# Optimization experiments

Measured on AMD Instinct MI355X. Metric: run time of the kernel, lower is better.

Reference implementation:

```python
import jax, jax.numpy as jnp
import numpy as np

IN_FEATURES = 4096
OUT_FEATURES = 11008
GROUPSIZE = 128


def setup_inputs() -> dict:
    key = jax.random.key(0)
    k_x, k_w, k_s, k_z = jax.random.split(key, 4)
    x = jax.random.normal(k_x, (4, 2048, IN_FEATURES), dtype=jnp.float32)
    # each int32 word packs 8 int4 nibbles along the in_features axis
    packed_weight = jax.random.randint(
        k_w, (IN_FEATURES // 8, OUT_FEATURES), 0, 2147483647, dtype=jnp.int32
    )
    n_groups = IN_FEATURES // GROUPSIZE
    scales = jax.random.uniform(k_s, (OUT_FEATURES, n_groups), dtype=jnp.float32)
    zeros = jax.random.uniform(k_z, (OUT_FEATURES, n_groups), dtype=jnp.float32)
    return {
        "x": x,
        "packed_weight": packed_weight,
        "scales": scales,
        "zeros": zeros,
        "groupsize": GROUPSIZE,
    }


def reference(x, packed_weight, scales, zeros, groupsize):
    # Unpack int4 nibbles: element i of in_features lives in packed_weight[i//8],
    # nibble (i % 8) (little-endian nibble order).
    in_features = packed_weight.shape[0] * 8
    shifts = (jnp.arange(8, dtype=jnp.int32) * 4)  # [8]
    q = (packed_weight[:, None, :] >> shifts[None, :, None]) & 0xF  # [in//8, 8, out]
    q = q.reshape(in_features, -1).astype(jnp.float32)  # [in, out]
    # Per-group dequant: w = (q - zero) * scale, groups along in_features.
    s = jnp.repeat(scales.T, groupsize, axis=0)  # [in, out]
    z = jnp.repeat(zeros.T, groupsize, axis=0)   # [in, out]
    w = (q - z) * s
    return jnp.einsum("bsi,io->bso", x, w)
```

## Files before the change

kernel.cpp:

```cpp
#include <hip/hip_runtime.h>


#define M_DIM 8192
#define K_DIM 4096
#define N_DIM 11008
#define BM 256
#define BN 256
#define BK 64
#define NKT (K_DIM / BK)

typedef unsigned short u16;
typedef __bf16 bf16x8 __attribute__((ext_vector_type(8)));
typedef float floatx4 __attribute__((ext_vector_type(4)));
typedef u16 u16x8 __attribute__((ext_vector_type(8)));
typedef u16 u16x4 __attribute__((ext_vector_type(4)));

typedef __attribute__((address_space(1))) const void* gcvp;
typedef __attribute__((address_space(3))) void* svp;

static __device__ __forceinline__ u16 f2b(float f) {
  union { float f; unsigned u; } v;
  v.f = f;
  unsigned r = v.u + 0x7FFFu + ((v.u >> 16) & 1u);
  return (u16)(r >> 16);
}

__global__ __launch_bounds__(256) void cvt_x_kernel(const float* __restrict__ x,
                                                    u16* __restrict__ xb) {
  int i = blockIdx.x * 256 + threadIdx.x;
  const int n4 = (M_DIM * K_DIM) / 4;
  const int stride = 2048 * 256;
  for (; i < n4; i += stride) {
    const float4 v = reinterpret_cast<const float4*>(x)[i];
    u16x4 r;
    r[0] = f2b(v.x); r[1] = f2b(v.y); r[2] = f2b(v.z); r[3] = f2b(v.w);
    reinterpret_cast<u16x4*>(xb)[i] = r;
  }
}

__global__ __launch_bounds__(256) void dequant_w_kernel(const int* __restrict__ pw,
                                                        const float* __restrict__ sc,
                                                        const float* __restrict__ zr,
                                                        u16* __restrict__ wbt) {
  __shared__ int tile[64][65];
  const int t = threadIdx.x;
  const int o0 = blockIdx.x * 64;
  const int kw0 = blockIdx.y * 64;
#pragma unroll
  for (int r = 0; r < 16; ++r) {
    const int kw = r * 4 + (t >> 6);
    const int o = t & 63;
    tile[kw][o] = pw[(kw0 + kw) * N_DIM + o0 + o];
  }
  __syncthreads();
  const int kwl = t & 63;
  const int g = (kw0 + kwl) >> 4;
  const int obase = (t >> 6) * 16;
  for (int it = 0; it < 16; ++it) {
    const int ol = obase + it;
    const int o = o0 + ol;
    const float s = sc[o * 32 + g];
    const float z = zr[o * 32 + g];
    const float b = -z * s;
    const int word = tile[kwl][ol];
    u16x8 r;
#pragma unroll
    for (int j = 0; j < 8; ++j) {
      const float q = (float)((word >> (4 * j)) & 0xF);
      r[j] = f2b(fmaf(q, s, b));
    }
    *reinterpret_cast<u16x8*>(&wbt[(size_t)o * K_DIM + (size_t)(kw0 + kwl) * 8]) = r;
  }
}


#define WAITL0                                               \
  asm volatile("s_waitcnt lgkmcnt(0)" ::: "memory");         \
  __builtin_amdgcn_sched_barrier(0)
#define WAITV(n)                                             \
  asm volatile("s_waitcnt vmcnt(" #n ")" ::: "memory");      \
  __builtin_amdgcn_sched_barrier(0)
#define BAR __builtin_amdgcn_s_barrier()

__global__ __launch_bounds__(512, 2) void gemm_kernel(const u16* __restrict__ xb,
                                                      const u16* __restrict__ wbt,
                                                      float* __restrict__ out) {
  __shared__ __align__(16) u16 lds[2][2][BM * BK];

  const int tid = threadIdx.x;
  const int w = tid >> 6;
  const int l = tid & 63;
  const int wm = w >> 2;
  const int wn = w & 3;

  const int bid = blockIdx.x;
  const int wg = (bid & 7) * 172 + (bid >> 3);
  const int NT = N_DIM / BN;
  const int m0 = (wg / NT) * BM;
  const int n0 = (wg % NT) * BN;

  const int sr = tid >> 3;
  const int scc = ((tid & 7) ^ (sr & 7)) * 8;
  const u16* srcA = xb + (size_t)(m0 + sr) * K_DIM + scc;
  const u16* srcB = wbt + (size_t)(n0 + sr) * K_DIM + scc;

#define STAGEQ(buf, op, q, t)                                                  \
  __builtin_amdgcn_global_load_lds(                                            \
      gcvp(((op) ? srcB : srcA) + (size_t)((q) * 64) * K_DIM + (t) * 64),      \
      svp(&lds[buf][op][((q) * 64 + w * 8) * 64]), 16, 0, 0)

  const int swz = ((l >> 4) ^ (l & 7)) * 8;
  const int baseA = (wm * 128 + (l & 15)) * 64 + swz;
  const int baseB = 16384 + (wn * 64 + (l & 15)) * 64 + swz;
  const u16* lp = &lds[0][0][0];

  bf16x8 a[4][2], b0[2][2], b1[2][2];

#define LDA(cb, S)                                                                      \
  do {                                                                                  \
    _Pragma("unroll") for (int _m = 0; _m < 4; ++_m) {                                  \
      const int _e = (cb) + baseA + ((S) * 4 + _m) * 1024;                              \
      a[_m][0] = *reinterpret_cast<const bf16x8*>(&lp[_e]);                             \
      a[_m][1] = *reinterpret_cast<const bf16x8*>(&lp[_e ^ 32]);                        \
    }                                                                                   \
  } while (0)
#define LDB(cb, BA, U)                                                                  \
  do {                                                                                  \
    _Pragma("unroll") for (int _n = 0; _n < 2; ++_n) {                                  \
      const int _e = (cb) + baseB + ((U) * 2 + _n) * 1024;                              \
      BA[_n][0] = *reinterpret_cast<const bf16x8*>(&lp[_e]);                            \
      BA[_n][1] = *reinterpret_cast<const bf16x8*>(&lp[_e ^ 32]);                       \
    }                                                                                   \
  } while (0)

  floatx4 acc[8][4] = {};

#define QMFMA(S, BA, U)                                                                 \
  do {                                                                                  \
    __builtin_amdgcn_s_setprio(1);                                                     \
    _Pragma("unroll") for (int _m = 0; _m < 4; ++_m)                                    \
      _Pragma("unroll") for (int _n = 0; _n < 2; ++_n)                                  \
        _Pragma("unroll") for (int _k = 0; _k < 2; ++_k)                                \
          acc[(S) * 4 + _m][(U) * 2 + _n] = __builtin_amdgcn_mfma_f32_16x16x32_bf16(    \
              a[_m][_k], BA[_n][_k], acc[(S) * 4 + _m][(U) * 2 + _n], 0, 0, 0);         \
    __builtin_amdgcn_s_setprio(0);                                                     \
  } while (0)

  STAGEQ(0, 0, 0, 0); STAGEQ(0, 0, 1, 0); STAGEQ(0, 0, 2, 0); STAGEQ(0, 0, 3, 0);
  STAGEQ(0, 1, 0, 0); STAGEQ(0, 1, 1, 0); STAGEQ(0, 1, 2, 0); STAGEQ(0, 1, 3, 0);
  STAGEQ(1, 0, 0, 1); STAGEQ(1, 0, 1, 1); STAGEQ(1, 0, 2, 1); STAGEQ(1, 0, 3, 1);
  STAGEQ(1, 1, 0, 1); STAGEQ(1, 1, 1, 1);
  WAITV(6);
  BAR;

#pragma unroll 2
  for (int t = 0; t < NKT - 2; ++t) {
    const int buf = t & 1;
    const int sb = buf ^ 1;
    const int cb = buf * 32768;
    LDA(cb, 0);
    LDB(cb, b0, 0);
    STAGEQ(sb, 1, 2, t + 1); STAGEQ(sb, 1, 3, t + 1);
    WAITV(6); BAR; WAITL0; BAR;
    QMFMA(0, b0, 0);
    LDB(cb, b1, 1);
    STAGEQ(buf, 0, 0, t + 2); STAGEQ(buf, 0, 2, t + 2);
    WAITV(6); BAR; WAITL0; BAR;
    QMFMA(0, b1, 1);
    LDA(cb, 1);
    STAGEQ(buf, 1, 0, t + 2); STAGEQ(buf, 1, 1, t + 2);
    WAITV(6); BAR; WAITL0; BAR;
    QMFMA(1, b0, 0);
    STAGEQ(buf, 0, 1, t + 2); STAGEQ(buf, 0, 3, t + 2);
    WAITV(6); BAR;
    QMFMA(1, b1, 1);
  }

  {
    const int cb = 0;
    LDA(cb, 0);
    LDB(cb, b0, 0);
    STAGEQ(1, 1, 2, NKT - 1); STAGEQ(1, 1, 3, NKT - 1);
    WAITV(6); BAR; WAITL0; BAR;
    QMFMA(0, b0, 0);
    LDB(cb, b1, 1);
    WAITV(4); BAR; WAITL0; BAR;
    QMFMA(0, b1, 1);
    LDA(cb, 1);
    WAITV(2); BAR; WAITL0; BAR;
    QMFMA(1, b0, 0);
    WAITV(0); BAR;
    QMFMA(1, b1, 1);
  }
  {
    const int cb = 32768;
    LDA(cb, 0);
    LDB(cb, b0, 0);
    WAITL0;
    QMFMA(0, b0, 0);
    LDB(cb, b1, 1);
    WAITL0;
    QMFMA(0, b1, 1);
    LDA(cb, 1);
    WAITL0;
    QMFMA(1, b0, 0);
    QMFMA(1, b1, 1);
  }

  const int orow0 = m0 + wm * 128 + (l >> 4) * 4;
  const int ocol0 = n0 + wn * 64 + (l & 15);
#pragma unroll
  for (int mi = 0; mi < 8; ++mi)
#pragma unroll
    for (int j = 0; j < 4; ++j) {
      float* op = out + (size_t)(orow0 + mi * 16 + j) * N_DIM + ocol0;
#pragma unroll
      for (int ni = 0; ni < 4; ++ni) op[ni * 16] = acc[mi][ni][j];
    }
}

__global__ __launch_bounds__(256) void gemm_naive(const float* __restrict__ x,
                                                  const int* __restrict__ pw,
                                                  const float* __restrict__ sc,
                                                  const float* __restrict__ zr,
                                                  float* __restrict__ out) {
  const int idx = blockIdx.x * 256 + threadIdx.x;
  if (idx >= M_DIM * N_DIM) return;
  const int m = idx / N_DIM, o = idx % N_DIM;
  const float* xr = x + (size_t)m * K_DIM;
  float acc = 0.f;
  for (int g = 0; g < 32; ++g) {
    const float s = sc[o * 32 + g];
    const float z = zr[o * 32 + g];
    const float b = -z * s;
    for (int kw = g * 16; kw < g * 16 + 16; ++kw) {
      const int word = pw[kw * N_DIM + o];
#pragma unroll
      for (int j = 0; j < 8; ++j) {
        const float q = (float)((word >> (4 * j)) & 0xF);
        acc += xr[kw * 8 + j] * fmaf(q, s, b);
      }
    }
  }
  out[idx] = acc;
}

extern "C" void kernel_launch(void* const* d_in, const int* in_sizes, int n_in,
                              void* d_out, int out_size, void* d_ws, size_t ws_size,
                              hipStream_t stream) {
  (void)in_sizes; (void)n_in; (void)out_size;
  const float* x = (const float*)d_in[0];
  const int* pw = (const int*)d_in[1];
  const float* sc = (const float*)d_in[2];
  const float* zr = (const float*)d_in[3];
  float* out = (float*)d_out;

  const size_t need = ((size_t)M_DIM * K_DIM + (size_t)N_DIM * K_DIM) * 2;
  if (ws_size >= need) {
    u16* xb = (u16*)d_ws;
    u16* wbt = xb + (size_t)M_DIM * K_DIM;
    cvt_x_kernel<<<2048, 256, 0, stream>>>(x, xb);
    dequant_w_kernel<<<dim3(N_DIM / 64, (K_DIM / 8) / 64), 256, 0, stream>>>(pw, sc, zr, wbt);
    gemm_kernel<<<(M_DIM / BM) * (N_DIM / BN), 512, 0, stream>>>(xb, wbt, out);
  } else {
    gemm_naive<<<(M_DIM * N_DIM + 255) / 256, 256, 0, stream>>>(x, pw, sc, zr, out);
  }
}
```

Measured before the change: 718.3 us.

## Restructure K-loop pipeline to one barrier per tile with one-ahead staging

Replaces the two-tile-ahead staging schedule, which used a wait and barrier pair at each of four phases, with a one-tile-ahead schedule. The new loop does a single full vmem wait and barrier at the top of each iteration, then issues all stages for the next tile interleaved with LDS reads and MFMAs. The epilogue tile is also removed from the unrolled tail. This cuts synchronisation overhead but reduces prefetch distance, so global-load latency may be less well hidden.

```diff
diff --git a/kernel.cpp b/kernel.cpp
--- a/kernel.cpp
+++ b/kernel.cpp
@@ -146,54 +146,35 @@
     __builtin_amdgcn_s_setprio(0);                                                     \
   } while (0)
 
+  STAGEQ(0, 1, 2, 0); STAGEQ(0, 1, 3, 0);
+  STAGEQ(0, 1, 0, 0); STAGEQ(0, 1, 1, 0);
   STAGEQ(0, 0, 0, 0); STAGEQ(0, 0, 1, 0); STAGEQ(0, 0, 2, 0); STAGEQ(0, 0, 3, 0);
-  STAGEQ(0, 1, 0, 0); STAGEQ(0, 1, 1, 0); STAGEQ(0, 1, 2, 0); STAGEQ(0, 1, 3, 0);
-  STAGEQ(1, 0, 0, 1); STAGEQ(1, 0, 1, 1); STAGEQ(1, 0, 2, 1); STAGEQ(1, 0, 3, 1);
-  STAGEQ(1, 1, 0, 1); STAGEQ(1, 1, 1, 1);
-  WAITV(6);
-  BAR;
 
 #pragma unroll 2
-  for (int t = 0; t < NKT - 2; ++t) {
+  for (int t = 0; t < NKT - 1; ++t) {
     const int buf = t & 1;
     const int sb = buf ^ 1;
     const int cb = buf * 32768;
+    WAITV(0); BAR;
+    STAGEQ(sb, 1, 2, t + 1); STAGEQ(sb, 1, 3, t + 1);
     LDA(cb, 0);
     LDB(cb, b0, 0);
-    STAGEQ(sb, 1, 2, t + 1); STAGEQ(sb, 1, 3, t + 1);
-    WAITV(6); BAR; WAITL0; BAR;
+    WAITL0;
     QMFMA(0, b0, 0);
+    STAGEQ(sb, 1, 0, t + 1); STAGEQ(sb, 1, 1, t + 1); STAGEQ(sb, 0, 0, t + 1);
     LDB(cb, b1, 1);
-    STAGEQ(buf, 0, 0, t + 2); STAGEQ(buf, 0, 2, t + 2);
-    WAITV(6); BAR; WAITL0; BAR;
+    WAITL0;
     QMFMA(0, b1, 1);
+    STAGEQ(sb, 0, 1, t + 1); STAGEQ(sb, 0, 2, t + 1); STAGEQ(sb, 0, 3, t + 1);
     LDA(cb, 1);
-    STAGEQ(buf, 1, 0, t + 2); STAGEQ(buf, 1, 1, t + 2);
-    WAITV(6); BAR; WAITL0; BAR;
+    WAITL0;
     QMFMA(1, b0, 0);
-    STAGEQ(buf, 0, 1, t + 2); STAGEQ(buf, 0, 3, t + 2);
-    WAITV(6); BAR;
     QMFMA(1, b1, 1);
   }
 
-  {
-    const int cb = 0;
-    LDA(cb, 0);
-    LDB(cb, b0, 0);
-    STAGEQ(1, 1, 2, NKT - 1); STAGEQ(1, 1, 3, NKT - 1);
-    WAITV(6); BAR; WAITL0; BAR;
-    QMFMA(0, b0, 0);
-    LDB(cb, b1, 1);
-    WAITV(4); BAR; WAITL0; BAR;
-    QMFMA(0, b1, 1);
-    LDA(cb, 1);
-    WAITV(2); BAR; WAITL0; BAR;
-    QMFMA(1, b0, 0);
-    WAITV(0); BAR;
-    QMFMA(1, b1, 1);
-  }
   {
     const int cb = 32768;
+    WAITV(0); BAR;
     LDA(cb, 0);
     LDB(cb, b0, 0);
     WAITL0;
```

Result: slower. 782.4 us (+8.9%).
